# Performance work log

Hardware: AMD Instinct MI355X
Metric: run time of the kernel (lower is better)

## Reference

```python
import jax, jax.numpy as jnp
import numpy as np

B, S, HID = 2, 1024, 2048
NH, HD = 16, 128          # num_heads, head_dim
NN = 16                   # num_neighbors
RHID = 1024               # hidden_size // compression_factor
CTX = 2                   # context_size
SCALE = HD ** -0.5


def setup_inputs() -> dict:
    key = jax.random.key(0)
    ks = jax.random.split(key, 6)
    return {
        "hidden_states": jax.random.normal(ks[0], (B, S, HID), jnp.float32),
        "ext_hidden_states": jax.random.normal(ks[1], (B, S, NN, RHID), jnp.float32),
        # weights stored (in_features, out_features)
        "Wq": jax.random.normal(ks[2], (HID, NH * HD), jnp.float32) * 0.02,
        "Wk": jax.random.normal(ks[3], (RHID, NH * HD), jnp.float32) * 0.02,
        "Wv": jax.random.normal(ks[4], (RHID, NH * HD), jnp.float32) * 0.02,
        "Wo": jax.random.normal(ks[5], (NH * HD, HID), jnp.float32) * 0.02,
    }


def _repeat_neighbors(n, seq_len):
    # n: [B, S, H, NN, HD] -> [B, S, H, CTX*NN, HD], gathering a ctx window
    # of previous positions' neighbors for each query (clamped at 0).
    context = jnp.clip(
        jnp.arange(seq_len)[:, None] + jnp.arange(-CTX + 1, 1)[None, :],
        0, seq_len - 1)                     # [S, CTX]
    n = jnp.moveaxis(n, 1, 2)               # [B, H, S, NN, HD]
    n = n[:, :, context]                    # [B, H, S, CTX, NN, HD]
    n = n.reshape(n.shape[0], n.shape[1], seq_len, -1, HD)
    return jnp.moveaxis(n, 1, 2)            # [B, S, H, CTX*NN, HD]


def reference(hidden_states, ext_hidden_states, Wq, Wk, Wv, Wo):
    b, s, hid = hidden_states.shape
    nn_ = ext_hidden_states.shape[2]
    q = (hidden_states @ Wq) * SCALE
    q = q.reshape(b, s, NH, HD)                         # [B,S,H,D]
    # note: original views [B,S,NN,H*D] as [B,S,H,NN,D] (pure reshape)
    k = (ext_hidden_states @ Wk).reshape(b, s, NH, nn_, HD)
    v = (ext_hidden_states @ Wv).reshape(b, s, NH, nn_, HD)
    if CTX > 1:
        k = _repeat_neighbors(k, s)                     # [B,S,H,I,D]
        v = _repeat_neighbors(v, s)
    attn = jnp.einsum('bqhd,bqhid->bhqi', q, k)
    attn = jax.nn.softmax(attn.astype(jnp.float32), axis=-1).astype(q.dtype)
    out = jnp.einsum('bhqi,bqhid->bqhd', attn, v)
    out = out.reshape(b, s, hid) @ Wo
    return out + hidden_states
```

## Files before the change

kernel.cpp:

```cpp
#include <hip/hip_runtime.h>
#include <stdint.h>

#define DEVI __device__ __forceinline__

typedef __bf16 bf16x8 __attribute__((ext_vector_type(8)));
typedef float f32x4 __attribute__((ext_vector_type(4)));
typedef unsigned short u16;

static constexpr float SCALE_ = 0.08838834764831845f;

DEVI u16 f2bf(float f) {
  uint32_t u = __float_as_uint(f);
  u += 0x7fffu + ((u >> 16) & 1u);
  return (u16)(u >> 16);
}
DEVI float bfraw2f(uint32_t hi) { return __uint_as_float(hi); }

__global__ void k_cast(const float* __restrict__ in, u16* __restrict__ out) {
  int i = blockIdx.x * blockDim.x + threadIdx.x;
  float4 v = ((const float4*)in)[i];
  ushort4 o;
  o.x = f2bf(v.x); o.y = f2bf(v.y); o.z = f2bf(v.z); o.w = f2bf(v.w);
  ((ushort4*)out)[i] = o;
}

__global__ void k_transpose_cast(const float* __restrict__ in, u16* __restrict__ out,
                                 int R, int C) {
  __shared__ float t[32][33];
  int tx = threadIdx.x & 31, ty = threadIdx.x >> 5;
  int c0 = blockIdx.x << 5, r0 = blockIdx.y << 5;
  #pragma unroll
  for (int rr = 0; rr < 32; rr += 8) t[ty + rr][tx] = in[(r0 + ty + rr) * C + c0 + tx];
  __syncthreads();
  #pragma unroll
  for (int rr = 0; rr < 32; rr += 8) out[(c0 + ty + rr) * R + r0 + tx] = f2bf(t[tx][ty + rr]);
}

DEVI void gl_lds16(const u16* g, u16* l) {
  __builtin_amdgcn_global_load_lds((const __attribute__((address_space(1))) void*)g,
                                   (__attribute__((address_space(3))) void*)l, 16, 0, 0);
}

template<bool OUTF32, bool RESID>
__global__ __launch_bounds__(256, 2) void k_gemm(
    const u16* __restrict__ A, const u16* __restrict__ Bt, void* __restrict__ Cv,
    const float* __restrict__ resid, int M, int N, int K, float scale) {
  __shared__ __align__(16) u16 As[128 * 32];
  __shared__ __align__(16) u16 Bs[128 * 32];
  const int nbn = N >> 7;
  const int bm = blockIdx.x / nbn, bn = blockIdx.x - bm * nbn;
  const int tid = threadIdx.x, w = tid >> 6, lane = tid & 63;
  const int wr = w >> 1, wc = w & 1;
  const int lr = lane & 15, kg = lane >> 4;

  const u16* Ab = A + (size_t)bm * 128 * K;
  const u16* Bb = Bt + (size_t)bn * 128 * K;

  f32x4 acc[4][4] = {};

  for (int k0 = 0; k0 < K; k0 += 32) {
    #pragma unroll
    for (int t = 0; t < 2; t++) {
      const int ub = w * 128 + t * 64;
      const int u = ub + lane;
      const size_t go = (size_t)(u >> 2) * K + k0 + (u & 3) * 8;
      gl_lds16(Ab + go, &As[ub * 8]);
      gl_lds16(Bb + go, &Bs[ub * 8]);
    }
    __syncthreads();
    bf16x8 af[4], bv[4];
    #pragma unroll
    for (int m = 0; m < 4; m++) af[m] = *(const bf16x8*)&As[(wr * 64 + m * 16 + lr) * 32 + kg * 8];
    #pragma unroll
    for (int n = 0; n < 4; n++) bv[n] = *(const bf16x8*)&Bs[(wc * 64 + n * 16 + lr) * 32 + kg * 8];
    #pragma unroll
    for (int m = 0; m < 4; m++)
      #pragma unroll
      for (int n = 0; n < 4; n++)
        acc[m][n] = __builtin_amdgcn_mfma_f32_16x16x32_bf16(af[m], bv[n], acc[m][n], 0, 0, 0);
    __syncthreads();
  }

  const int r0 = bm * 128 + wr * 64 + kg * 4;
  const int c0 = bn * 128 + wc * 64 + lr;
  if constexpr (OUTF32) {
    float* Co = (float*)Cv;
    #pragma unroll
    for (int m = 0; m < 4; m++)
      #pragma unroll
      for (int n = 0; n < 4; n++)
        #pragma unroll
        for (int j = 0; j < 4; j++) {
          size_t idx = (size_t)(r0 + m * 16 + j) * N + (c0 + n * 16);
          float v = acc[m][n][j] * scale;
          if constexpr (RESID) v += resid[idx];
          Co[idx] = v;
        }
  } else {
    u16* Co = (u16*)Cv;
    #pragma unroll
    for (int m = 0; m < 4; m++)
      #pragma unroll
      for (int n = 0; n < 4; n++)
        #pragma unroll
        for (int j = 0; j < 4; j++) {
          size_t idx = (size_t)(r0 + m * 16 + j) * N + (c0 + n * 16);
          Co[idx] = f2bf(acc[m][n][j] * scale);
        }
  }
}

__global__ __launch_bounds__(128, 2) void k_attn(
    const u16* __restrict__ Q, const u16* __restrict__ Kb,
    const u16* __restrict__ Vb, u16* __restrict__ O) {
  __shared__ __align__(16) u16 Kl[2][32][136];
  __shared__ __align__(16) u16 Vl[2][32][136];
  __shared__ __align__(16) u16 ql[2 * 128];
  const int tid = threadIdx.x;
  const int hg = blockIdx.x & 7;
  const int s = blockIdx.x >> 3;
  const int sm1 = s ? s - 1 : 0;

  #pragma unroll
  for (int it = 0; it < 8; it++) {
    int e = (it * 128 + tid) * 8;
    int hh = e >> 12;
    int rem = e & 4095;
    int ifull = rem >> 7, d = rem & 127;
    int ctx = ifull >> 4, i = ifull & 15;
    int h = hg * 2 + hh;
    size_t g = ((size_t)(ctx ? s : sm1) * 16 + h) * 2048 + i * 128 + d;
    *(bf16x8*)&Kl[hh][ifull][d] = *(const bf16x8*)&Kb[g];
    *(bf16x8*)&Vl[hh][ifull][d] = *(const bf16x8*)&Vb[g];
  }
  if (tid < 32) *(bf16x8*)&ql[tid * 8] = *(const bf16x8*)&Q[(size_t)s * 2048 + hg * 256 + tid * 8];
  __syncthreads();

  const int w = tid >> 6, lane = tid & 63;
  const int ni = lane & 31, dh = lane >> 5;
  float sc = 0.f;
  #pragma unroll
  for (int t = 0; t < 8; t++) {
    bf16x8 kv = *(const bf16x8*)&Kl[w][ni][dh * 64 + t * 8];
    bf16x8 qv = *(const bf16x8*)&ql[w * 128 + dh * 64 + t * 8];
    #pragma unroll
    for (int j = 0; j < 8; j++) sc += (float)kv[j] * (float)qv[j];
  }
  sc += __shfl_xor(sc, 32);
  float mx = sc;
  #pragma unroll
  for (int m_ = 16; m_; m_ >>= 1) mx = fmaxf(mx, __shfl_xor(mx, m_));
  float ex = __expf(sc - mx);
  float sm = ex;
  #pragma unroll
  for (int m_ = 16; m_; m_ >>= 1) sm += __shfl_xor(sm, m_);
  float pr = ex / sm;

  float o0 = 0.f, o1 = 0.f;
  #pragma unroll
  for (int i2 = 0; i2 < 32; i2++) {
    float pi = __shfl(pr, i2);
    uint32_t vv = *(const uint32_t*)&Vl[w][i2][lane * 2];
    o0 += pi * bfraw2f(vv << 16);
    o1 += pi * bfraw2f(vv & 0xffff0000u);
  }
  int h = hg * 2 + w;
  uint32_t ov = (uint32_t)f2bf(o0) | ((uint32_t)f2bf(o1) << 16);
  *(uint32_t*)&O[((size_t)s * 16 + h) * 128 + lane * 2] = ov;
}

extern "C" void kernel_launch(void* const* d_in, const int* in_sizes, int n_in,
                              void* d_out, int out_size, void* d_ws, size_t ws_size,
                              hipStream_t stream) {
  (void)in_sizes; (void)n_in; (void)out_size; (void)ws_size;
  const float* hs  = (const float*)d_in[0];
  const float* ext = (const float*)d_in[1];
  const float* Wq  = (const float*)d_in[2];
  const float* Wk  = (const float*)d_in[3];
  const float* Wv  = (const float*)d_in[4];
  const float* Wo  = (const float*)d_in[5];
  float* out = (float*)d_out;

  char* p = (char*)d_ws;
  auto alloc = [&](size_t elems) {
    u16* r = (u16*)p;
    p += ((elems * 2 + 255) & ~(size_t)255);
    return r;
  };
  u16* hs_bf  = alloc(4ull << 20);
  u16* ext_bf = alloc(32ull << 20);
  u16* Wq_t   = alloc(4ull << 20);
  u16* Wk_t   = alloc(2ull << 20);
  u16* Wv_t   = alloc(2ull << 20);
  u16* Wo_t   = alloc(4ull << 20);
  u16* Qb     = alloc(4ull << 20);
  u16* Ob     = alloc(4ull << 20);
  u16* Kbuf   = alloc(32ull << 20);
  u16* Vbuf   = alloc(32ull << 20);

  k_cast<<<4096, 256, 0, stream>>>(hs, hs_bf);
  k_cast<<<32768, 256, 0, stream>>>(ext, ext_bf);
  k_transpose_cast<<<dim3(64, 64), 256, 0, stream>>>(Wq, Wq_t, 2048, 2048);
  k_transpose_cast<<<dim3(64, 32), 256, 0, stream>>>(Wk, Wk_t, 1024, 2048);
  k_transpose_cast<<<dim3(64, 32), 256, 0, stream>>>(Wv, Wv_t, 1024, 2048);
  k_transpose_cast<<<dim3(64, 64), 256, 0, stream>>>(Wo, Wo_t, 2048, 2048);

  k_gemm<false, false><<<16 * 16, 256, 0, stream>>>(hs_bf, Wq_t, Qb, nullptr,
                                                    2048, 2048, 2048, SCALE_);
  for (int b = 0; b < 2; b++) {
    const u16* extb = ext_bf + (size_t)b * 16384 * 1024;
    k_gemm<false, false><<<128 * 16, 256, 0, stream>>>(extb, Wk_t, Kbuf, nullptr,
                                                       16384, 2048, 1024, 1.0f);
    k_gemm<false, false><<<128 * 16, 256, 0, stream>>>(extb, Wv_t, Vbuf, nullptr,
                                                       16384, 2048, 1024, 1.0f);
    k_attn<<<1024 * 8, 128, 0, stream>>>(Qb + (size_t)b * 1024 * 2048, Kbuf, Vbuf,
                                         Ob + (size_t)b * 1024 * 2048);
  }
  k_gemm<true, true><<<16 * 16, 256, 0, stream>>>(Ob, Wo_t, out, hs,
                                                  2048, 2048, 2048, 1.0f);
}
```

Measured before the change: 744.0 us.

## Fuse K and V projections into one pipelined 256x256-tile GEMM kernel

Concatenates the transposed Wk and Wv into a single weight matrix. The two K/V projection GEMMs become one N=4096 GEMM, so the ext activations are read once per batch. A new kernel does this GEMM with 256x256 tiles, 512 threads, a double-buffered 128KB LDS with XOR swizzling, global-to-LDS async loads interleaved with MFMA, and priority hints. The attention kernel now reads K and V from the interleaved buffer at a 4096 stride. Ob reuses the hs_bf workspace. The large LDS footprint limits occupancy to one block per CU and relies on hand-placed waitcnt and barriers being correct.

```diff
diff --git a/kernel.cpp b/kernel.cpp
--- a/kernel.cpp
+++ b/kernel.cpp
@@ -83,36 +83,115 @@
 
   const int r0 = bm * 128 + wr * 64 + kg * 4;
   const int c0 = bn * 128 + wc * 64 + lr;
-  if constexpr (OUTF32) {
-    float* Co = (float*)Cv;
-    #pragma unroll
-    for (int m = 0; m < 4; m++)
-      #pragma unroll
-      for (int n = 0; n < 4; n++)
+  #pragma unroll
+  for (int m = 0; m < 4; m++)
+    #pragma unroll
+    for (int n = 0; n < 4; n++)
+      #pragma unroll
+      for (int j = 0; j < 4; j++) {
+        size_t idx = (size_t)(r0 + m * 16 + j) * N + (c0 + n * 16);
+        float v = acc[m][n][j] * scale;
+        if constexpr (OUTF32) {
+          if constexpr (RESID) v += resid[idx];
+          ((float*)Cv)[idx] = v;
+        } else {
+          ((u16*)Cv)[idx] = f2bf(v);
+        }
+      }
+}
+
+__global__ __launch_bounds__(512, 2) void k_kv256(
+    const u16* __restrict__ A, const u16* __restrict__ Bt, u16* __restrict__ C) {
+  constexpr int K = 1024, NT = K / 64, LDC = 4096;
+  __shared__ __align__(16) u16 lds[65536];
+  char* ldsc = (char*)lds;
+  const int tid = threadIdx.x, w = tid >> 6, lane = tid & 63;
+  const int wr = w >> 2, wc = w & 3;
+  const int lr = lane & 15, kg = lane >> 4, x3 = lr & 7;
+  const int bm = blockIdx.x >> 4, bn = blockIdx.x & 15;
+
+  const int u0 = tid, u1 = 512 + tid;
+  const int r0s = u0 >> 3, r1s = u1 >> 3;
+  const int ro0 = r0s * K + ((u0 & 7) ^ (r0s & 7)) * 8;
+  const int ro1 = r1s * K + ((u1 & 7) ^ (r1s & 7)) * 8;
+  const u16* Ab = A + (size_t)bm * 256 * K;
+  const u16* Bb = Bt + (size_t)bn * 256 * K;
+
+  auto stage = [&](int db2, int q, int k64) {
+    const int h = q & 1;
+    const u16* base = (q >= 2) ? Bb : Ab;
+    uint32_t dst = ((q >= 2) ? 65536u : 0u) + (uint32_t)(db2 * 2 + h) * 16384u
+                   + (uint32_t)w * 1024u;
+    const size_t tb = (size_t)h * 128 * K + k64;
+    gl_lds16(base + tb + ro0, (u16*)(ldsc + dst));
+    gl_lds16(base + tb + ro1, (u16*)(ldsc + dst + 8192u));
+  };
+
+  f32x4 acc[8][4] = {};
+
+  #pragma unroll
+  for (int q = 0; q < 4; ++q) stage(0, q, 0);
+  __builtin_amdgcn_sched_barrier(0);
+
+  for (int kt = 0; kt < NT; ++kt) {
+    const int c = kt & 1;
+    const int nk64 = (kt + 1 < NT ? kt + 1 : kt) * 64;
+    __builtin_amdgcn_sched_barrier(0);
+    __builtin_amdgcn_s_barrier();
+    __builtin_amdgcn_sched_barrier(0);
+    stage(c ^ 1, 0, nk64);
+    __builtin_amdgcn_sched_barrier(0);
+    asm volatile("s_waitcnt vmcnt(2)" ::: "memory");
+    __builtin_amdgcn_sched_barrier(0);
+    __builtin_amdgcn_s_barrier();
+    __builtin_amdgcn_sched_barrier(0);
+
+    const uint32_t a_base = (uint32_t)(c * 2 + wr) * 16384u;
+    const uint32_t b_base = 65536u + (uint32_t)(c * 2 + (wc >> 1)) * 16384u;
+    #pragma unroll
+    for (int q = 0; q < 4; ++q) {
+      if (q > 0) { stage(c ^ 1, q, nk64); __builtin_amdgcn_sched_barrier(0); }
+      const int mh = q >> 1, nh = q & 1;
+      bf16x8 af[4][2], bfr[2][2];
+      #pragma unroll
+      for (int m = 0; m < 4; ++m)
         #pragma unroll
-        for (int j = 0; j < 4; j++) {
-          size_t idx = (size_t)(r0 + m * 16 + j) * N + (c0 + n * 16);
-          float v = acc[m][n][j] * scale;
-          if constexpr (RESID) v += resid[idx];
-          Co[idx] = v;
-        }
-  } else {
-    u16* Co = (u16*)Cv;
-    #pragma unroll
-    for (int m = 0; m < 4; m++)
-      #pragma unroll
-      for (int n = 0; n < 4; n++)
+        for (int ks = 0; ks < 2; ++ks)
+          af[m][ks] = *(const bf16x8*)(ldsc + a_base + (mh * 64 + m * 16 + lr) * 128
+                                       + ((((ks << 2) | kg) ^ x3) << 4));
+      #pragma unroll
+      for (int n = 0; n < 2; ++n)
         #pragma unroll
-        for (int j = 0; j < 4; j++) {
-          size_t idx = (size_t)(r0 + m * 16 + j) * N + (c0 + n * 16);
-          Co[idx] = f2bf(acc[m][n][j] * scale);
-        }
-  }
+        for (int ks = 0; ks < 2; ++ks)
+          bfr[n][ks] = *(const bf16x8*)(ldsc + b_base
+                                        + ((wc & 1) * 64 + (nh * 2 + n) * 16 + lr) * 128
+                                        + ((((ks << 2) | kg) ^ x3) << 4));
+      __builtin_amdgcn_s_setprio(1);
+      #pragma unroll
+      for (int m = 0; m < 4; ++m)
+        #pragma unroll
+        for (int n = 0; n < 2; ++n)
+          #pragma unroll
+          for (int ks = 0; ks < 2; ++ks)
+            acc[mh * 4 + m][nh * 2 + n] = __builtin_amdgcn_mfma_f32_16x16x32_bf16(
+                af[m][ks], bfr[n][ks], acc[mh * 4 + m][nh * 2 + n], 0, 0, 0);
+      __builtin_amdgcn_s_setprio(0);
+    }
+  }
+
+  const int gr0 = bm * 256 + wr * 128 + kg * 4;
+  const int gc0 = bn * 256 + wc * 64 + lr;
+  #pragma unroll
+  for (int m = 0; m < 8; ++m)
+    #pragma unroll
+    for (int n = 0; n < 4; ++n)
+      #pragma unroll
+      for (int j = 0; j < 4; ++j)
+        C[(size_t)(gr0 + m * 16 + j) * LDC + gc0 + n * 16] = f2bf(acc[m][n][j]);
 }
 
 __global__ __launch_bounds__(128, 2) void k_attn(
-    const u16* __restrict__ Q, const u16* __restrict__ Kb,
-    const u16* __restrict__ Vb, u16* __restrict__ O) {
+    const u16* __restrict__ Q, const u16* __restrict__ KV, u16* __restrict__ O) {
   __shared__ __align__(16) u16 Kl[2][32][136];
   __shared__ __align__(16) u16 Vl[2][32][136];
   __shared__ __align__(16) u16 ql[2 * 128];
@@ -129,9 +208,9 @@
     int ifull = rem >> 7, d = rem & 127;
     int ctx = ifull >> 4, i = ifull & 15;
     int h = hg * 2 + hh;
-    size_t g = ((size_t)(ctx ? s : sm1) * 16 + h) * 2048 + i * 128 + d;
-    *(bf16x8*)&Kl[hh][ifull][d] = *(const bf16x8*)&Kb[g];
-    *(bf16x8*)&Vl[hh][ifull][d] = *(const bf16x8*)&Vb[g];
+    size_t g = ((size_t)(ctx ? s : sm1) * 16 + h) * 4096 + i * 128 + d;
+    *(bf16x8*)&Kl[hh][ifull][d] = *(const bf16x8*)&KV[g];
+    *(bf16x8*)&Vl[hh][ifull][d] = *(const bf16x8*)&KV[g + 2048];
   }
   if (tid < 32) *(bf16x8*)&ql[tid * 8] = *(const bf16x8*)&Q[(size_t)s * 2048 + hg * 256 + tid * 8];
   __syncthreads();
@@ -190,32 +269,27 @@
   u16* hs_bf  = alloc(4ull << 20);
   u16* ext_bf = alloc(32ull << 20);
   u16* Wq_t   = alloc(4ull << 20);
-  u16* Wk_t   = alloc(2ull << 20);
-  u16* Wv_t   = alloc(2ull << 20);
+  u16* Wkv_t  = alloc(8ull << 20);
   u16* Wo_t   = alloc(4ull << 20);
   u16* Qb     = alloc(4ull << 20);
-  u16* Ob     = alloc(4ull << 20);
-  u16* Kbuf   = alloc(32ull << 20);
-  u16* Vbuf   = alloc(32ull << 20);
+  u16* KVbuf  = alloc(64ull << 20);
+  u16* Ob     = hs_bf;
 
   k_cast<<<4096, 256, 0, stream>>>(hs, hs_bf);
   k_cast<<<32768, 256, 0, stream>>>(ext, ext_bf);
   k_transpose_cast<<<dim3(64, 64), 256, 0, stream>>>(Wq, Wq_t, 2048, 2048);
-  k_transpose_cast<<<dim3(64, 32), 256, 0, stream>>>(Wk, Wk_t, 1024, 2048);
-  k_transpose_cast<<<dim3(64, 32), 256, 0, stream>>>(Wv, Wv_t, 1024, 2048);
+  k_transpose_cast<<<dim3(64, 32), 256, 0, stream>>>(Wk, Wkv_t, 1024, 2048);
+  k_transpose_cast<<<dim3(64, 32), 256, 0, stream>>>(Wv, Wkv_t + (2048ull * 1024), 1024, 2048);
   k_transpose_cast<<<dim3(64, 64), 256, 0, stream>>>(Wo, Wo_t, 2048, 2048);
 
-  k_gemm<false, false><<<16 * 16, 256, 0, stream>>>(hs_bf, Wq_t, Qb, nullptr,
-                                                    2048, 2048, 2048, SCALE_);
+  k_gemm<false, false><<<256, 256, 0, stream>>>(hs_bf, Wq_t, Qb, nullptr,
+                                                2048, 2048, 2048, SCALE_);
   for (int b = 0; b < 2; b++) {
     const u16* extb = ext_bf + (size_t)b * 16384 * 1024;
-    k_gemm<false, false><<<128 * 16, 256, 0, stream>>>(extb, Wk_t, Kbuf, nullptr,
-                                                       16384, 2048, 1024, 1.0f);
-    k_gemm<false, false><<<128 * 16, 256, 0, stream>>>(extb, Wv_t, Vbuf, nullptr,
-                                                       16384, 2048, 1024, 1.0f);
-    k_attn<<<1024 * 8, 128, 0, stream>>>(Qb + (size_t)b * 1024 * 2048, Kbuf, Vbuf,
+    k_kv256<<<64 * 16, 512, 0, stream>>>(extb, Wkv_t, KVbuf);
+    k_attn<<<1024 * 8, 128, 0, stream>>>(Qb + (size_t)b * 1024 * 2048, KVbuf,
                                          Ob + (size_t)b * 1024 * 2048);
   }
-  k_gemm<true, true><<<16 * 16, 256, 0, stream>>>(Ob, Wo_t, out, hs,
-                                                  2048, 2048, 2048, 1.0f);
-}
+  k_gemm<true, true><<<256, 256, 0, stream>>>(Ob, Wo_t, out, hs,
+                                              2048, 2048, 2048, 1.0f);
+}
```

New measurement: 651.9 us. -12.4%, faster.
